# Performance work log

Measured on AMD Instinct MI355X. Metric: run time of the kernel, lower is better.

Reference implementation:

```python
import jax, jax.numpy as jnp
import numpy as np

N = 16384      # total points
B = 8          # point clouds in batch
PER = N // B   # points per cloud (batch ids sorted in blocks)
M = 4096       # sampled centers (ratio 0.25, strided sampler -> batch-aligned)
K = 64         # max_num_neighbors
R = 0.25       # ball-query radius
C_IN = 128
HID = 256
C_OUT = 256


def setup_inputs() -> dict:
    key = jax.random.key(0)
    k1, k2, k3, k4, k5 = jax.random.split(key, 5)
    x = jax.random.normal(k1, (N, C_IN), dtype=jnp.float32)
    pos = jax.random.uniform(k2, (N, 3), dtype=jnp.float32)  # unit cube
    batch = jnp.repeat(jnp.arange(B, dtype=jnp.int32), PER)  # sorted block batch ids
    lframes = jax.random.normal(k3, (N, 3, 3), dtype=jnp.float32)
    W1 = jax.random.normal(k4, (2 * C_IN + 3, HID), dtype=jnp.float32) * 0.05
    b1 = jnp.zeros((HID,), dtype=jnp.float32)
    W2 = jax.random.normal(k5, (HID, C_OUT), dtype=jnp.float32) * 0.05
    b2 = jnp.zeros((C_OUT,), dtype=jnp.float32)
    return {"x": x, "pos": pos, "batch": batch, "lframes": lframes,
            "W1": W1, "b1": b1, "W2": W2, "b2": b2}


def _ball_query(pos, batch, idx):
    """radius(pos, pos[idx], R, batch, batch[idx], max_num_neighbors=K).
    Returns fixed-size neighbor indices [M, K] + validity mask [M, K]."""
    pos_c = pos[idx]                                  # [M, 3]
    # squared distances via gemm trick (avoid [M, N, 3] broadcast)
    d2 = ((pos_c ** 2).sum(-1)[:, None]
          + (pos ** 2).sum(-1)[None, :]
          - 2.0 * pos_c @ pos.T)                      # [M, N]
    valid = (d2 <= R * R) & (batch[idx][:, None] == batch[None, :])
    score = jnp.where(valid, -d2, -jnp.inf)
    vals, nbr = jax.lax.top_k(score, K)               # K nearest within ball
    return nbr, jnp.isfinite(vals)


def reference(x, pos, batch, lframes, W1, b1, W2, b2):
    # center sampler: strided subsample (batch-aligned since batch is block-sorted)
    idx = jnp.arange(0, N, N // M)                    # [M]
    nbr, vmask = _ball_query(pos, batch, idx)         # [M, K]

    pos_dst = pos[idx]                                # [M, 3]
    x_dst = x[idx]                                    # [M, C_IN]
    lframes_dst = lframes[idx]                        # [M, 3, 3]

    # EdgeConv: per-edge message MLP([x_src, x_dst, lframe_dst @ (pos_src - pos_dst)])
    rel = pos[nbr] - pos_dst[:, None, :]              # [M, K, 3]
    rel_loc = jnp.einsum('mij,mkj->mki', lframes_dst, rel)  # rotate into dst frame
    feats = jnp.concatenate([
        x[nbr],                                        # [M, K, C_IN]
        jnp.broadcast_to(x_dst[:, None, :], (M, K, C_IN)),
        rel_loc,
    ], axis=-1)                                        # [M, K, 2*C_IN+3]

    h = jax.nn.relu(feats @ W1 + b1)                   # [M, K, HID]
    msg = h @ W2 + b2                                  # [M, K, C_OUT]

    # masked max aggregation over valid neighbors
    msg = jnp.where(vmask[..., None], msg, -jnp.inf)
    out = msg.max(axis=1)                              # [M, C_OUT]
    out = jnp.where(jnp.isfinite(out), out, 0.0)
    return out, pos_dst, batch[idx], lframes_dst
```

## Files before the change

kernel.cpp:

```cpp
#include <hip/hip_runtime.h>
#include <hip/hip_bf16.h>

#define N_PTS 16384
#define PER   2048
#define M_CTR 4096
#define KNB   64
#define C_IN  128
#define HID   256
#define C_OUT 256

typedef unsigned short u16;
typedef unsigned int u32;
typedef __attribute__((ext_vector_type(8))) short s8v;
typedef __attribute__((ext_vector_type(4))) float f4v;
typedef __attribute__((ext_vector_type(4))) unsigned int u4v;

static __device__ __forceinline__ u16 f2bf(float f) {
    union { float f; unsigned int i; } v; v.f = f;
    unsigned int r = v.i + 0x7FFFu + ((v.i >> 16) & 1u);
    return (u16)(r >> 16);
}

__global__ __launch_bounds__(256) void ballq_kernel(
        const float* __restrict__ pos, int* __restrict__ nbr, int* __restrict__ cnt,
        const float* __restrict__ W1, const float* __restrict__ W2,
        u16* __restrict__ W1aT, u16* __restrict__ W1bT, u16* __restrict__ W2T) {
    __shared__ float cd2[1024];
    __shared__ int   cidx[1024];
    __shared__ int   s_n;
    int m = blockIdx.x, tid = threadIdx.x;

    if (m < 256) {
        int gid = m * 256 + tid;
        int cc = gid >> 8, k = gid & 255;
        W2T[gid] = f2bf(W2[k * 256 + cc]);
        if (gid < 32768) {
            int c1 = gid >> 7, k1 = gid & 127;
            W1aT[gid] = f2bf(W1[k1 * 256 + c1]);
            W1bT[gid] = f2bf(W1[(k1 + 128) * 256 + c1]);
        }
    }

    int c = m * 4;
    int base = (m >> 9) << 11;
    int ln = tid & 63;
    if (tid == 0) s_n = 0;
    __syncthreads();
    float cx = pos[c * 3 + 0], cy = pos[c * 3 + 1], cz = pos[c * 3 + 2];
    float A = __fadd_rn(__fadd_rn(__fmul_rn(cx, cx), __fmul_rn(cy, cy)), __fmul_rn(cz, cz));
    float c2x = __fmul_rn(2.0f, cx);
    float c2y = __fmul_rn(2.0f, cy);
    float c2z = __fmul_rn(2.0f, cz);
    for (int s = 0; s < 8; ++s) {
        int j = base + tid + (s << 8);
        float px = pos[j * 3 + 0], py = pos[j * 3 + 1], pz = pos[j * 3 + 2];
        float B = __fadd_rn(__fadd_rn(__fmul_rn(px, px), __fmul_rn(py, py)), __fmul_rn(pz, pz));
        float C = __fmaf_rn(c2z, pz, __fmaf_rn(c2y, py, __fmul_rn(c2x, px)));
        float d2 = __fsub_rn(__fadd_rn(A, B), C);
        bool hit = (d2 <= 0.0625f);
        unsigned long long mk = __ballot(hit);
        int nb = __popcll(mk & ((1ull << ln) - 1ull));
        int tot = __popcll(mk);
        int bidx = 0;
        if (ln == 0 && tot) bidx = atomicAdd(&s_n, tot);
        bidx = __shfl(bidx, 0, 64);
        if (hit) {
            int a = bidx + nb;
            if (a < 1024) { cd2[a] = d2; cidx[a] = j; }
        }
    }
    __syncthreads();
    int V = s_n < 1024 ? s_n : 1024;
    if (V <= KNB) {
        if (tid < KNB) nbr[m * KNB + tid] = (tid < V) ? cidx[tid] : c;
        if (tid == 0) cnt[m] = V;
    } else {
        for (int e = tid; e < V; e += 256) {
            float de = cd2[e]; int ie = cidx[e];
            int rank = 0;
            for (int q = 0; q < V; ++q) {
                float dq = cd2[q];
                rank += (dq < de) || (dq == de && cidx[q] < ie);
            }
            if (rank < KNB) nbr[m * KNB + rank] = cidx[e];
        }
        if (tid == 0) cnt[m] = KNB;
    }
}

__global__ __launch_bounds__(256) void gemm_xw_kernel(
        const float* __restrict__ x, const u16* __restrict__ W1aT, const u16* __restrict__ W1bT,
        const float* __restrict__ b1, u16* __restrict__ u_out, float* __restrict__ v_out) {
    __shared__ u16 x_lds[64 * 136];
    int blk = blockIdx.x, tid = threadIdx.x;
    int mode = blk >= 256 ? 1 : 0;
    int bb = mode ? blk - 256 : blk;
    const u16* WT = mode ? W1bT : W1aT;
    {
        int r = tid >> 2, q = tid & 3;
        int xrow = bb * 64 + r;
        if (mode) xrow *= 4;
        const float* xp = x + xrow * C_IN + q * 32;
        u16* dst = x_lds + r * 136 + q * 32;
        for (int i = 0; i < 8; ++i) {
            f4v f = *(const f4v*)(xp + i * 4);
            dst[i * 4 + 0] = f2bf(f[0]);
            dst[i * 4 + 1] = f2bf(f[1]);
            dst[i * 4 + 2] = f2bf(f[2]);
            dst[i * 4 + 3] = f2bf(f[3]);
        }
    }
    __syncthreads();
    int lane = tid & 63, w = tid >> 6;
    int quad = lane >> 4, l16 = lane & 15;
    int cb = w * 64;
    f4v acc[4][4] = {};
    for (int k0 = 0; k0 < 128; k0 += 32) {
        s8v a[4], b[4];
        for (int rt = 0; rt < 4; ++rt)
            a[rt] = *(const s8v*)&x_lds[(rt * 16 + l16) * 136 + k0 + quad * 8];
        for (int ct = 0; ct < 4; ++ct)
            b[ct] = *(const s8v*)(WT + (cb + ct * 16 + l16) * 128 + k0 + quad * 8);
        for (int rt = 0; rt < 4; ++rt)
            for (int ct = 0; ct < 4; ++ct)
                acc[rt][ct] = __builtin_amdgcn_mfma_f32_16x16x32_bf16(a[rt], b[ct], acc[rt][ct], 0, 0, 0);
    }
    for (int rt = 0; rt < 4; ++rt)
        for (int ct = 0; ct < 4; ++ct)
            for (int g = 0; g < 4; ++g) {
                int row = rt * 16 + quad * 4 + g;
                int col = cb + ct * 16 + l16;
                float val = acc[rt][ct][g];
                int orow = bb * 64 + row;
                if (mode == 0) u_out[orow * 256 + col] = f2bf(val);
                else           v_out[orow * 256 + col] = val + b1[col];
            }
}

__global__ __launch_bounds__(512, 4) void edge_kernel(
        const u16* __restrict__ u, const float* __restrict__ v,
        const u16* __restrict__ W2T, const float* __restrict__ W1,
        const float* __restrict__ b2, const float* __restrict__ pos,
        const float* __restrict__ lframes, const int* __restrict__ batch,
        const int* __restrict__ nbrg, const int* __restrict__ cnt,
        float* __restrict__ out0, float* __restrict__ out_pos,
        float* __restrict__ out_batch, float* __restrict__ out_lf) {
    __shared__ u16   h_lds[64 * 264];
    __shared__ float w1c_lds[768];
    __shared__ f4v   relc_lds[8][64];
    __shared__ u16   nbr_lds[8][64];

    int blk = blockIdx.x, tid = threadIdx.x;
    int m0 = ((blk & 7) << 9) | ((blk >> 3) << 3);

    int lane = tid & 63, w = tid >> 6;
    int quad = lane >> 4, l16 = lane & 15;
    int cb = w * 32;

    s8v bfrag[4][2];
    #pragma unroll
    for (int k0 = 0; k0 < 4; ++k0)
        #pragma unroll
        for (int ct = 0; ct < 2; ++ct)
            bfrag[k0][ct] = *(const s8v*)(W2T + (cb + ct * 16 + l16) * 256 + k0 * 32 + quad * 8);

    for (int i = tid; i < 768; i += 512) w1c_lds[i] = W1[65536 + i];
    {
        int pr = tid >> 6, t = tid & 63;
        int mm = m0 + pr, cc = mm * 4;
        int j = nbrg[mm * KNB + t];
        nbr_lds[pr][t] = (u16)j;
        float rx = pos[j * 3 + 0] - pos[cc * 3 + 0];
        float ry = pos[j * 3 + 1] - pos[cc * 3 + 1];
        float rz = pos[j * 3 + 2] - pos[cc * 3 + 2];
        const float* lf = lframes + cc * 9;
        f4v r;
        r[0] = lf[0] * rx + lf[1] * ry + lf[2] * rz;
        r[1] = lf[3] * rx + lf[4] * ry + lf[5] * rz;
        r[2] = lf[6] * rx + lf[7] * ry + lf[8] * rz;
        r[3] = 0.0f;
        relc_lds[pr][t] = r;
    }
    if (tid >= 256 && tid < 384) {
        int g = (tid - 256) >> 4, t = tid & 15;
        int mm = m0 + g, cc = mm * 4;
        if (t < 3)            out_pos[mm * 3 + t] = pos[cc * 3 + t];
        else if (t == 3)      out_batch[mm] = (float)batch[cc];
        else if (t < 13)      out_lf[mm * 9 + (t - 4)] = lframes[cc * 9 + (t - 4)];
    }

    int co = (tid & 31) * 8;
    int rs = tid >> 5;
    __syncthreads();

    for (int p = 0; p < 8; ++p) {
        int cvp = cnt[m0 + p];
        {
            const float* vp = v + (m0 + p) * 256 + co;
            f4v vq0 = *(const f4v*)vp;
            f4v vq1 = *(const f4v*)(vp + 4);
            f4v wa0 = *(const f4v*)&w1c_lds[co],       wa1 = *(const f4v*)&w1c_lds[co + 4];
            f4v wb0 = *(const f4v*)&w1c_lds[256 + co], wb1 = *(const f4v*)&w1c_lds[256 + co + 4];
            f4v wc0 = *(const f4v*)&w1c_lds[512 + co], wc1 = *(const f4v*)&w1c_lds[512 + co + 4];
            u4v uu[4];
            f4v rr[4];
            #pragma unroll
            for (int i2 = 0; i2 < 4; ++i2) {
                int rl = rs + i2 * 16;
                int j = (int)nbr_lds[p][rl];
                uu[i2] = *(const u4v*)(u + j * 256 + co);
                rr[i2] = relc_lds[p][rl];
            }
            #pragma unroll
            for (int i2 = 0; i2 < 4; ++i2) {
                int rl = rs + i2 * 16;
                f4v r = rr[i2];
                float p8[8];
                #pragma unroll
                for (int e = 0; e < 8; ++e) {
                    u32 bits = (e & 1) ? (uu[i2][e >> 1] & 0xFFFF0000u) : (uu[i2][e >> 1] << 16);
                    float va = (e < 4) ? vq0[e] : vq1[e - 4];
                    float a0 = (e < 4) ? wa0[e] : wa1[e - 4];
                    float b0 = (e < 4) ? wb0[e] : wb1[e - 4];
                    float c0 = (e < 4) ? wc0[e] : wc1[e - 4];
                    float pre = fmaf(r[0], a0, fmaf(r[1], b0, fmaf(r[2], c0,
                                  va + __uint_as_float(bits))));
                    p8[e] = fmaxf(pre, 0.0f);
                }
                u4v pk;
                #pragma unroll
                for (int d = 0; d < 4; ++d)
                    pk[d] = __builtin_amdgcn_perm(__float_as_uint(p8[2 * d + 1]),
                                                  __float_as_uint(p8[2 * d]), 0x07060302u);
                *(u4v*)&h_lds[rl * 264 + co] = pk;
            }
        }
        __syncthreads();

        s8v bs[4][2];
        #pragma unroll
        for (int kk = 0; kk < 4; ++kk)
            #pragma unroll
            for (int ct = 0; ct < 2; ++ct)
                bs[kk][ct] = *(const s8v*)(W2T + (cb + ct * 16 + l16) * 256 + (4 + kk) * 32 + quad * 8);
        f4v acc[4][2] = {};
        #pragma unroll
        for (int k0 = 0; k0 < 4; ++k0) {
            s8v a[4];
            #pragma unroll
            for (int rt = 0; rt < 4; ++rt)
                a[rt] = *(const s8v*)&h_lds[(rt * 16 + l16) * 264 + k0 * 32 + quad * 8];
            #pragma unroll
            for (int rt = 0; rt < 4; ++rt)
                #pragma unroll
                for (int ct = 0; ct < 2; ++ct)
                    acc[rt][ct] = __builtin_amdgcn_mfma_f32_16x16x32_bf16(a[rt], bfrag[k0][ct], acc[rt][ct], 0, 0, 0);
        }
        #pragma unroll
        for (int kk = 0; kk < 4; ++kk) {
            int k0 = 4 + kk;
            s8v a[4];
            #pragma unroll
            for (int rt = 0; rt < 4; ++rt)
                a[rt] = *(const s8v*)&h_lds[(rt * 16 + l16) * 264 + k0 * 32 + quad * 8];
            #pragma unroll
            for (int rt = 0; rt < 4; ++rt)
                #pragma unroll
                for (int ct = 0; ct < 2; ++ct)
                    acc[rt][ct] = __builtin_amdgcn_mfma_f32_16x16x32_bf16(a[rt], bs[kk][ct], acc[rt][ct], 0, 0, 0);
        }
        int mout = m0 + p;
        #pragma unroll
        for (int ct = 0; ct < 2; ++ct) {
            float mx = -__builtin_inff();
            #pragma unroll
            for (int rt = 0; rt < 4; ++rt)
                #pragma unroll
                for (int g = 0; g < 4; ++g) {
                    int row = rt * 16 + quad * 4 + g;
                    float val = acc[rt][ct][g];
                    if (row < cvp) mx = fmaxf(mx, val);
                }
            mx = fmaxf(mx, __shfl_xor(mx, 16, 64));
            mx = fmaxf(mx, __shfl_xor(mx, 32, 64));
            if (lane < 16)
                out0[mout * 256 + cb + ct * 16 + l16] = mx + b2[cb + ct * 16 + l16];
        }
        if (p < 7) __syncthreads();
    }
}

extern "C" void kernel_launch(void* const* d_in, const int* in_sizes, int n_in,
                              void* d_out, int out_size, void* d_ws, size_t ws_size,
                              hipStream_t stream) {
    const float* x       = (const float*)d_in[0];
    const float* pos     = (const float*)d_in[1];
    const int*   batch   = (const int*)d_in[2];
    const float* lframes = (const float*)d_in[3];
    const float* W1      = (const float*)d_in[4];
    const float* b1      = (const float*)d_in[5];
    const float* W2      = (const float*)d_in[6];
    const float* b2      = (const float*)d_in[7];

    float* out       = (float*)d_out;
    float* out_pos   = out + M_CTR * 256;
    float* out_batch = out_pos + M_CTR * 3;
    float* out_lf    = out_batch + M_CTR;

    char* ws = (char*)d_ws;
    u16*   u_ws = (u16*)(ws);
    float* v_ws = (float*)(ws + 8388608);
    u16*   W1aT = (u16*)(ws + 12582912);
    u16*   W1bT = (u16*)(ws + 12648448);
    u16*   W2T  = (u16*)(ws + 12713984);
    int*   nbr  = (int*)(ws + 12845056);
    int*   cntp = (int*)(ws + 13893632);

    hipLaunchKernelGGL(ballq_kernel, dim3(M_CTR), dim3(256), 0, stream,
                       pos, nbr, cntp, W1, W2, W1aT, W1bT, W2T);
    hipLaunchKernelGGL(gemm_xw_kernel, dim3(320), dim3(256), 0, stream,
                       x, W1aT, W1bT, b1, u_ws, v_ws);
    hipLaunchKernelGGL(edge_kernel, dim3(512), dim3(512), 0, stream,
                       u_ws, v_ws, W2T, W1, b2, pos, lframes, batch, nbr, cntp,
                       out, out_pos, out_batch, out_lf);
}
```

Baseline: 162.2 us.

## Assign one wavefront per ball-query center instead of one block

The ball-query kernel now handles four centers per 256-thread block, one 64-lane wavefront each, with per-wave LDS candidate buffers. The shared atomic counter and block-wide barriers are replaced by a wave-local running count built from ballot and popcount. This removes block-level synchronisation and LDS atomics and cuts the grid from 4096 to 1024 blocks. In exchange, each wave scans 2048 points serially in 32 steps, and the rank sort for overfull balls runs over 64 lanes instead of 256, so crowded centers take longer. The weight-transpose prologue still runs in the first 256 blocks.

New measurement: 190.4 us. 1.17x slower.

```diff
diff --git a/kernel.cpp b/kernel.cpp
--- a/kernel.cpp
+++ b/kernel.cpp
@@ -25,13 +25,12 @@
         const float* __restrict__ pos, int* __restrict__ nbr, int* __restrict__ cnt,
         const float* __restrict__ W1, const float* __restrict__ W2,
         u16* __restrict__ W1aT, u16* __restrict__ W1bT, u16* __restrict__ W2T) {
-    __shared__ float cd2[1024];
-    __shared__ int   cidx[1024];
-    __shared__ int   s_n;
-    int m = blockIdx.x, tid = threadIdx.x;
-
-    if (m < 256) {
-        int gid = m * 256 + tid;
+    __shared__ float cd2[4][1024];
+    __shared__ int   cidx[4][1024];
+    int blk = blockIdx.x, tid = threadIdx.x;
+
+    if (blk < 256) {
+        int gid = blk * 256 + tid;
         int cc = gid >> 8, k = gid & 255;
         W2T[gid] = f2bf(W2[k * 256 + cc]);
         if (gid < 32768) {
@@ -41,18 +40,18 @@
         }
     }
 
+    int w = tid >> 6, ln = tid & 63;
+    int m = blk * 4 + w;
     int c = m * 4;
     int base = (m >> 9) << 11;
-    int ln = tid & 63;
-    if (tid == 0) s_n = 0;
-    __syncthreads();
     float cx = pos[c * 3 + 0], cy = pos[c * 3 + 1], cz = pos[c * 3 + 2];
     float A = __fadd_rn(__fadd_rn(__fmul_rn(cx, cx), __fmul_rn(cy, cy)), __fmul_rn(cz, cz));
     float c2x = __fmul_rn(2.0f, cx);
     float c2y = __fmul_rn(2.0f, cy);
     float c2z = __fmul_rn(2.0f, cz);
-    for (int s = 0; s < 8; ++s) {
-        int j = base + tid + (s << 8);
+    int n = 0;
+    for (int s = 0; s < 32; ++s) {
+        int j = base + ln + (s << 6);
         float px = pos[j * 3 + 0], py = pos[j * 3 + 1], pz = pos[j * 3 + 2];
         float B = __fadd_rn(__fadd_rn(__fmul_rn(px, px), __fmul_rn(py, py)), __fmul_rn(pz, pz));
         float C = __fmaf_rn(c2z, pz, __fmaf_rn(c2y, py, __fmul_rn(c2x, px)));
@@ -60,31 +59,27 @@
         bool hit = (d2 <= 0.0625f);
         unsigned long long mk = __ballot(hit);
         int nb = __popcll(mk & ((1ull << ln) - 1ull));
-        int tot = __popcll(mk);
-        int bidx = 0;
-        if (ln == 0 && tot) bidx = atomicAdd(&s_n, tot);
-        bidx = __shfl(bidx, 0, 64);
         if (hit) {
-            int a = bidx + nb;
-            if (a < 1024) { cd2[a] = d2; cidx[a] = j; }
-        }
-    }
-    __syncthreads();
-    int V = s_n < 1024 ? s_n : 1024;
+            int a = n + nb;
+            if (a < 1024) { cd2[w][a] = d2; cidx[w][a] = j; }
+        }
+        n += __popcll(mk);
+    }
+    int V = n < 1024 ? n : 1024;
     if (V <= KNB) {
-        if (tid < KNB) nbr[m * KNB + tid] = (tid < V) ? cidx[tid] : c;
-        if (tid == 0) cnt[m] = V;
+        if (ln < KNB) nbr[m * KNB + ln] = (ln < V) ? cidx[w][ln] : c;
+        if (ln == 0) cnt[m] = V;
     } else {
-        for (int e = tid; e < V; e += 256) {
-            float de = cd2[e]; int ie = cidx[e];
+        for (int e = ln; e < V; e += 64) {
+            float de = cd2[w][e]; int ie = cidx[w][e];
             int rank = 0;
             for (int q = 0; q < V; ++q) {
-                float dq = cd2[q];
-                rank += (dq < de) || (dq == de && cidx[q] < ie);
+                float dq = cd2[w][q];
+                rank += (dq < de) || (dq == de && cidx[w][q] < ie);
             }
-            if (rank < KNB) nbr[m * KNB + rank] = cidx[e];
-        }
-        if (tid == 0) cnt[m] = KNB;
+            if (rank < KNB) nbr[m * KNB + rank] = ie;
+        }
+        if (ln == 0) cnt[m] = KNB;
     }
 }
 
@@ -316,7 +311,7 @@
     int*   nbr  = (int*)(ws + 12845056);
     int*   cntp = (int*)(ws + 13893632);
 
-    hipLaunchKernelGGL(ballq_kernel, dim3(M_CTR), dim3(256), 0, stream,
+    hipLaunchKernelGGL(ballq_kernel, dim3(1024), dim3(256), 0, stream,
                        pos, nbr, cntp, W1, W2, W1aT, W1bT, W2T);
     hipLaunchKernelGGL(gemm_xw_kernel, dim3(320), dim3(256), 0, stream,
                        x, W1aT, W1bT, b1, u_ws, v_ws);
```

## Merge ball query and x@W1 GEMM into one launch with on-the-fly W1 conversion

Applied to the files above, without the earlier changes.

Combines the ball-query kernel and the x@W1 projection GEMM into a single launch, with disjoint block ranges doing each job and sharing one LDS buffer. The GEMM blocks now read fp32 W1 directly with strided loads and convert it to bf16 in registers, so the separate transposed bf16 copies of W1 are no longer needed. This removes one kernel launch and the serial dependency between the two stages, letting the GEMM overlap with the ball query. In exchange, W1 reads become uncoalesced strided scalar loads, and the GEMM tile is split into two passes to reduce register pressure.

Result: slower. 190.6 us (+17.5%).

```diff
diff --git a/kernel.cpp b/kernel.cpp
--- a/kernel.cpp
+++ b/kernel.cpp
@@ -21,120 +21,125 @@
     return (u16)(r >> 16);
 }
 
-__global__ __launch_bounds__(256) void ballq_kernel(
-        const float* __restrict__ pos, int* __restrict__ nbr, int* __restrict__ cnt,
+__global__ __launch_bounds__(256) void pre_kernel(
+        const float* __restrict__ pos, const float* __restrict__ x,
         const float* __restrict__ W1, const float* __restrict__ W2,
-        u16* __restrict__ W1aT, u16* __restrict__ W1bT, u16* __restrict__ W2T) {
-    __shared__ float cd2[1024];
-    __shared__ int   cidx[1024];
-    __shared__ int   s_n;
-    int m = blockIdx.x, tid = threadIdx.x;
-
-    if (m < 256) {
-        int gid = m * 256 + tid;
-        int cc = gid >> 8, k = gid & 255;
-        W2T[gid] = f2bf(W2[k * 256 + cc]);
-        if (gid < 32768) {
-            int c1 = gid >> 7, k1 = gid & 127;
-            W1aT[gid] = f2bf(W1[k1 * 256 + c1]);
-            W1bT[gid] = f2bf(W1[(k1 + 128) * 256 + c1]);
+        const float* __restrict__ b1,
+        int* __restrict__ nbr, int* __restrict__ cnt,
+        u16* __restrict__ W2T, u16* __restrict__ u_out, float* __restrict__ v_out) {
+    __shared__ __align__(16) char sh[64 * 136 * 2];
+    int blk = blockIdx.x, tid = threadIdx.x;
+
+    if (blk < 4096) {
+        float* cd2  = (float*)sh;
+        int*   cidx = (int*)(sh + 4096);
+        int*   s_np = (int*)(sh + 8192);
+        int m = blk;
+
+        if (m < 256) {
+            int gid = m * 256 + tid;
+            int cc = gid >> 8, k = gid & 255;
+            W2T[gid] = f2bf(W2[k * 256 + cc]);
+        }
+
+        int c = m * 4;
+        int base = (m >> 9) << 11;
+        int ln = tid & 63;
+        if (tid == 0) *s_np = 0;
+        __syncthreads();
+        float cx = pos[c * 3 + 0], cy = pos[c * 3 + 1], cz = pos[c * 3 + 2];
+        float A = __fadd_rn(__fadd_rn(__fmul_rn(cx, cx), __fmul_rn(cy, cy)), __fmul_rn(cz, cz));
+        float c2x = __fmul_rn(2.0f, cx);
+        float c2y = __fmul_rn(2.0f, cy);
+        float c2z = __fmul_rn(2.0f, cz);
+        for (int s = 0; s < 8; ++s) {
+            int j = base + tid + (s << 8);
+            float px = pos[j * 3 + 0], py = pos[j * 3 + 1], pz = pos[j * 3 + 2];
+            float B = __fadd_rn(__fadd_rn(__fmul_rn(px, px), __fmul_rn(py, py)), __fmul_rn(pz, pz));
+            float C = __fmaf_rn(c2z, pz, __fmaf_rn(c2y, py, __fmul_rn(c2x, px)));
+            float d2 = __fsub_rn(__fadd_rn(A, B), C);
+            bool hit = (d2 <= 0.0625f);
+            unsigned long long mk = __ballot(hit);
+            int nb = __popcll(mk & ((1ull << ln) - 1ull));
+            int tot = __popcll(mk);
+            int bidx = 0;
+            if (ln == 0 && tot) bidx = atomicAdd(s_np, tot);
+            bidx = __shfl(bidx, 0, 64);
+            if (hit) {
+                int a = bidx + nb;
+                if (a < 1024) { cd2[a] = d2; cidx[a] = j; }
+            }
+        }
+        __syncthreads();
+        int V = *s_np < 1024 ? *s_np : 1024;
+        if (V <= KNB) {
+            if (tid < KNB) nbr[m * KNB + tid] = (tid < V) ? cidx[tid] : c;
+            if (tid == 0) cnt[m] = V;
+        } else {
+            for (int e = tid; e < V; e += 256) {
+                float de = cd2[e]; int ie = cidx[e];
+                int rank = 0;
+                for (int q = 0; q < V; ++q) {
+                    float dq = cd2[q];
+                    rank += (dq < de) || (dq == de && cidx[q] < ie);
+                }
+                if (rank < KNB) nbr[m * KNB + rank] = cidx[e];
+            }
+            if (tid == 0) cnt[m] = KNB;
+        }
+    } else {
+        u16* x_lds = (u16*)sh;
+        int bb = blk - 4096;
+        int mode = bb >= 256 ? 1 : 0;
+        if (mode) bb -= 256;
+        {
+            int r = tid >> 2, q = tid & 3;
+            int xrow = bb * 64 + r;
+            if (mode) xrow *= 4;
+            const float* xp = x + xrow * C_IN + q * 32;
+            u16* dst = x_lds + r * 136 + q * 32;
+            for (int i = 0; i < 8; ++i) {
+                f4v f = *(const f4v*)(xp + i * 4);
+                dst[i * 4 + 0] = f2bf(f[0]);
+                dst[i * 4 + 1] = f2bf(f[1]);
+                dst[i * 4 + 2] = f2bf(f[2]);
+                dst[i * 4 + 3] = f2bf(f[3]);
+            }
+        }
+        __syncthreads();
+        int lane = tid & 63, w = tid >> 6;
+        int quad = lane >> 4, l16 = lane & 15;
+        int cb = w * 64;
+        for (int g = 0; g < 2; ++g) {
+            f4v acc[2][4] = {};
+            for (int k0 = 0; k0 < 128; k0 += 32) {
+                s8v a[2], b[4];
+                for (int rt = 0; rt < 2; ++rt)
+                    a[rt] = *(const s8v*)&x_lds[((g * 2 + rt) * 16 + l16) * 136 + k0 + quad * 8];
+                for (int ct = 0; ct < 4; ++ct) {
+                    const float* wp = W1 + ((mode ? 128 : 0) + k0 + quad * 8) * 256 + cb + ct * 16 + l16;
+                    u4v wv;
+                    #pragma unroll
+                    for (int d = 0; d < 4; ++d)
+                        wv[d] = (u32)f2bf(wp[(2 * d) * 256]) | ((u32)f2bf(wp[(2 * d + 1) * 256]) << 16);
+                    b[ct] = *(s8v*)&wv;
+                }
+                for (int rt = 0; rt < 2; ++rt)
+                    for (int ct = 0; ct < 4; ++ct)
+                        acc[rt][ct] = __builtin_amdgcn_mfma_f32_16x16x32_bf16(a[rt], b[ct], acc[rt][ct], 0, 0, 0);
+            }
+            for (int rt = 0; rt < 2; ++rt)
+                for (int ct = 0; ct < 4; ++ct)
+                    for (int gg = 0; gg < 4; ++gg) {
+                        int row = (g * 2 + rt) * 16 + quad * 4 + gg;
+                        int col = cb + ct * 16 + l16;
+                        float val = acc[rt][ct][gg];
+                        int orow = bb * 64 + row;
+                        if (mode == 0) u_out[orow * 256 + col] = f2bf(val);
+                        else           v_out[orow * 256 + col] = val + b1[col];
+                    }
         }
     }
-
-    int c = m * 4;
-    int base = (m >> 9) << 11;
-    int ln = tid & 63;
-    if (tid == 0) s_n = 0;
-    __syncthreads();
-    float cx = pos[c * 3 + 0], cy = pos[c * 3 + 1], cz = pos[c * 3 + 2];
-    float A = __fadd_rn(__fadd_rn(__fmul_rn(cx, cx), __fmul_rn(cy, cy)), __fmul_rn(cz, cz));
-    float c2x = __fmul_rn(2.0f, cx);
-    float c2y = __fmul_rn(2.0f, cy);
-    float c2z = __fmul_rn(2.0f, cz);
-    for (int s = 0; s < 8; ++s) {
-        int j = base + tid + (s << 8);
-        float px = pos[j * 3 + 0], py = pos[j * 3 + 1], pz = pos[j * 3 + 2];
-        float B = __fadd_rn(__fadd_rn(__fmul_rn(px, px), __fmul_rn(py, py)), __fmul_rn(pz, pz));
-        float C = __fmaf_rn(c2z, pz, __fmaf_rn(c2y, py, __fmul_rn(c2x, px)));
-        float d2 = __fsub_rn(__fadd_rn(A, B), C);
-        bool hit = (d2 <= 0.0625f);
-        unsigned long long mk = __ballot(hit);
-        int nb = __popcll(mk & ((1ull << ln) - 1ull));
-        int tot = __popcll(mk);
-        int bidx = 0;
-        if (ln == 0 && tot) bidx = atomicAdd(&s_n, tot);
-        bidx = __shfl(bidx, 0, 64);
-        if (hit) {
-            int a = bidx + nb;
-            if (a < 1024) { cd2[a] = d2; cidx[a] = j; }
-        }
-    }
-    __syncthreads();
-    int V = s_n < 1024 ? s_n : 1024;
-    if (V <= KNB) {
-        if (tid < KNB) nbr[m * KNB + tid] = (tid < V) ? cidx[tid] : c;
-        if (tid == 0) cnt[m] = V;
-    } else {
-        for (int e = tid; e < V; e += 256) {
-            float de = cd2[e]; int ie = cidx[e];
-            int rank = 0;
-            for (int q = 0; q < V; ++q) {
-                float dq = cd2[q];
-                rank += (dq < de) || (dq == de && cidx[q] < ie);
-            }
-            if (rank < KNB) nbr[m * KNB + rank] = cidx[e];
-        }
-        if (tid == 0) cnt[m] = KNB;
-    }
-}
-
-__global__ __launch_bounds__(256) void gemm_xw_kernel(
-        const float* __restrict__ x, const u16* __restrict__ W1aT, const u16* __restrict__ W1bT,
-        const float* __restrict__ b1, u16* __restrict__ u_out, float* __restrict__ v_out) {
-    __shared__ u16 x_lds[64 * 136];
-    int blk = blockIdx.x, tid = threadIdx.x;
-    int mode = blk >= 256 ? 1 : 0;
-    int bb = mode ? blk - 256 : blk;
-    const u16* WT = mode ? W1bT : W1aT;
-    {
-        int r = tid >> 2, q = tid & 3;
-        int xrow = bb * 64 + r;
-        if (mode) xrow *= 4;
-        const float* xp = x + xrow * C_IN + q * 32;
-        u16* dst = x_lds + r * 136 + q * 32;
-        for (int i = 0; i < 8; ++i) {
-            f4v f = *(const f4v*)(xp + i * 4);
-            dst[i * 4 + 0] = f2bf(f[0]);
-            dst[i * 4 + 1] = f2bf(f[1]);
-            dst[i * 4 + 2] = f2bf(f[2]);
-            dst[i * 4 + 3] = f2bf(f[3]);
-        }
-    }
-    __syncthreads();
-    int lane = tid & 63, w = tid >> 6;
-    int quad = lane >> 4, l16 = lane & 15;
-    int cb = w * 64;
-    f4v acc[4][4] = {};
-    for (int k0 = 0; k0 < 128; k0 += 32) {
-        s8v a[4], b[4];
-        for (int rt = 0; rt < 4; ++rt)
-            a[rt] = *(const s8v*)&x_lds[(rt * 16 + l16) * 136 + k0 + quad * 8];
-        for (int ct = 0; ct < 4; ++ct)
-            b[ct] = *(const s8v*)(WT + (cb + ct * 16 + l16) * 128 + k0 + quad * 8);
-        for (int rt = 0; rt < 4; ++rt)
-            for (int ct = 0; ct < 4; ++ct)
-                acc[rt][ct] = __builtin_amdgcn_mfma_f32_16x16x32_bf16(a[rt], b[ct], acc[rt][ct], 0, 0, 0);
-    }
-    for (int rt = 0; rt < 4; ++rt)
-        for (int ct = 0; ct < 4; ++ct)
-            for (int g = 0; g < 4; ++g) {
-                int row = rt * 16 + quad * 4 + g;
-                int col = cb + ct * 16 + l16;
-                float val = acc[rt][ct][g];
-                int orow = bb * 64 + row;
-                if (mode == 0) u_out[orow * 256 + col] = f2bf(val);
-                else           v_out[orow * 256 + col] = val + b1[col];
-            }
 }
 
 __global__ __launch_bounds__(512, 4) void edge_kernel(
@@ -310,16 +315,12 @@
     char* ws = (char*)d_ws;
     u16*   u_ws = (u16*)(ws);
     float* v_ws = (float*)(ws + 8388608);
-    u16*   W1aT = (u16*)(ws + 12582912);
-    u16*   W1bT = (u16*)(ws + 12648448);
     u16*   W2T  = (u16*)(ws + 12713984);
     int*   nbr  = (int*)(ws + 12845056);
     int*   cntp = (int*)(ws + 13893632);
 
-    hipLaunchKernelGGL(ballq_kernel, dim3(M_CTR), dim3(256), 0, stream,
-                       pos, nbr, cntp, W1, W2, W1aT, W1bT, W2T);
-    hipLaunchKernelGGL(gemm_xw_kernel, dim3(320), dim3(256), 0, stream,
-                       x, W1aT, W1bT, b1, u_ws, v_ws);
+    hipLaunchKernelGGL(pre_kernel, dim3(4416), dim3(256), 0, stream,
+                       pos, x, W1, W2, b1, nbr, cntp, W2T, u_ws, v_ws);
     hipLaunchKernelGGL(edge_kernel, dim3(512), dim3(512), 0, stream,
                        u_ws, v_ws, W2T, W1, b2, pos, lframes, batch, nbr, cntp,
                        out, out_pos, out_batch, out_lf);
```
